# Performance work log

Measured on AMD Instinct MI355X. Metric: run time of the kernel, lower is better.

Reference implementation:

```python
import jax, jax.numpy as jnp
import numpy as np

NUM_HEADS = 16
MAX_LEN = 1024  # RelativePositionalEncoding default


def setup_inputs() -> dict:
    key = jax.random.key(0)
    ks = jax.random.split(key, 12)
    S, B, E = 1024, 4, 1024
    hd = E // NUM_HEADS
    table = 2 * MAX_LEN - 1  # 2047
    mu = 1.0 / np.sqrt(E)
    def lin_w(k):
        return jax.random.uniform(k, (E, E), jnp.float32, -mu, mu)
    def lin_b(k):
        return jax.random.uniform(k, (E,), jnp.float32, -mu, mu)
    return {
        "query": jax.random.normal(ks[0], (S, B, E), jnp.float32),
        "key": jax.random.normal(ks[1], (S, B, E), jnp.float32),
        "value": jax.random.normal(ks[2], (S, B, E), jnp.float32),
        "Wq": lin_w(ks[3]), "bq": lin_b(ks[4]),
        "Wk": lin_w(ks[5]), "bk": lin_b(ks[6]),
        "Wv": lin_w(ks[7]), "bv": lin_b(ks[8]),
        "Wo": lin_w(ks[9]), "bo": lin_b(ks[10]),
        "rel_pos_table": jax.random.normal(ks[11], (table, hd), jnp.float32),
    }


def reference(query, key, value, Wq, bq, Wk, bk, Wv, bv, Wo, bo, rel_pos_table):
    S, B, E = query.shape
    H = NUM_HEADS
    hd = E // H
    scale = hd ** -0.5
    # eval-mode NoisyLoRALinear == plain linear with mu params
    q = (query @ Wq.T + bq).reshape(S, B, H, hd).transpose(1, 2, 0, 3) * scale  # [B,H,S,hd]
    k = (key @ Wk.T + bk).reshape(S, B, H, hd).transpose(1, 2, 0, 3)
    v = (value @ Wv.T + bv).reshape(S, B, H, hd).transpose(1, 2, 0, 3)
    content = jnp.einsum('bhsd,bhtd->bhst', q, k)  # [B,H,S,S]
    # relative position embeddings: rel_pos_table[final_mat] -> [S,S,hd]
    L = rel_pos_table.shape[0]  # 2*max_len - 1
    half = L // 2
    r = jnp.arange(S)
    dist = r[None, :] - r[:, None]
    idx = jnp.clip(dist, -half + 1, half - 1) + half - 1
    rel_emb = rel_pos_table[idx]  # [S,S,hd]
    pos = jnp.einsum('bhsd,std->bhst', q, rel_emb)
    attn = jax.nn.softmax(content + pos, axis=-1)
    out = jnp.einsum('bhst,bhtd->bhsd', attn, v)  # [B,H,S,hd]
    out = out.transpose(0, 2, 1, 3).reshape(B, S, E)
    out = out @ Wo.T + bo  # [B,S,E]
    return out.transpose(1, 0, 2)  # [S,B,E]
```

## Files before the change

### kernel.cpp

```cpp
#include <hip/hip_runtime.h>
#include <math.h>

#define S_LEN 1024
#define B_SZ 4
#define E_DIM 1024
#define H_NUM 16
#define HD 64
#define IDX_MAX 2044
#define NEG_BIG (-3.0e38f)

typedef __attribute__((ext_vector_type(8))) short s16x8;
typedef __attribute__((ext_vector_type(4))) float f32x4;

__device__ __forceinline__ unsigned short f2bf(float f) {
  union { float f; unsigned int u; } v; v.f = f;
  return (unsigned short)((v.u + 0x7FFFu + ((v.u >> 16) & 1u)) >> 16);
}
__device__ __forceinline__ float bf2f(unsigned short h) {
  union { unsigned int u; float f; } v; v.u = ((unsigned int)h) << 16;
  return v.f;
}
__device__ __forceinline__ void gload16(const void* g, void* l) {
  __builtin_amdgcn_global_load_lds(
      (const __attribute__((address_space(1))) void*)g,
      (__attribute__((address_space(3))) void*)l, 16, 0, 0);
}
__device__ __forceinline__ int clampg(int g) {
  return g < 0 ? 0 : (g > IDX_MAX ? IDX_MAX : g);
}

template <int CTRL>
__device__ __forceinline__ float dppror(float x) {
  union { float f; int i; } a, b;
  a.f = x;
  b.i = __builtin_amdgcn_update_dpp(a.i, a.i, CTRL, 0xF, 0xF, false);
  return b.f;
}
__device__ __forceinline__ float rmax16(float x) {
  x = fmaxf(x, dppror<0x128>(x));
  x = fmaxf(x, dppror<0x124>(x));
  x = fmaxf(x, dppror<0x122>(x));
  x = fmaxf(x, dppror<0x121>(x));
  return x;
}
__device__ __forceinline__ float rsum16(float x) {
  x += dppror<0x128>(x);
  x += dppror<0x124>(x);
  x += dppror<0x122>(x);
  x += dppror<0x121>(x);
  return x;
}

__global__ __launch_bounds__(256) void conv_all(
    const float* __restrict__ q, const float* __restrict__ k,
    const float* __restrict__ v, const float* __restrict__ wq,
    const float* __restrict__ wk, const float* __restrict__ wv,
    const float* __restrict__ wo, const float* __restrict__ tb,
    unsigned short* __restrict__ oq, unsigned short* __restrict__ ok,
    unsigned short* __restrict__ ov, unsigned short* __restrict__ owq,
    unsigned short* __restrict__ owk, unsigned short* __restrict__ owv,
    unsigned short* __restrict__ owo, unsigned short* __restrict__ otb)
{
  const int b = blockIdx.x;
  const float* src; unsigned short* dst; int n, lb;
  if (b < 2048)      { src = q;  dst = oq;  n = 4194304; lb = b; }
  else if (b < 4096) { src = k;  dst = ok;  n = 4194304; lb = b - 2048; }
  else if (b < 6144) { src = v;  dst = ov;  n = 4194304; lb = b - 4096; }
  else if (b < 6656) { src = wq; dst = owq; n = 1048576; lb = b - 6144; }
  else if (b < 7168) { src = wk; dst = owk; n = 1048576; lb = b - 6656; }
  else if (b < 7680) { src = wv; dst = owv; n = 1048576; lb = b - 7168; }
  else if (b < 8192) { src = wo; dst = owo; n = 1048576; lb = b - 7680; }
  else               { src = tb; dst = otb; n = 131008;  lb = b - 8192; }
  const int i = (lb * 256 + threadIdx.x) << 3;
  if (i >= n) return;
  const float4 a = *(const float4*)(src + i);
  const float4 c = *(const float4*)(src + i + 4);
  union { unsigned short us[8]; uint4 v4; } u;
  u.us[0] = f2bf(a.x); u.us[1] = f2bf(a.y); u.us[2] = f2bf(a.z); u.us[3] = f2bf(a.w);
  u.us[4] = f2bf(c.x); u.us[5] = f2bf(c.y); u.us[6] = f2bf(c.z); u.us[7] = f2bf(c.w);
  *(uint4*)(dst + i) = u.v4;
}

__global__ __launch_bounds__(256, 3) void qkv_mfma(
    const unsigned short* __restrict__ X0, const unsigned short* __restrict__ X1,
    const unsigned short* __restrict__ X2,
    const unsigned short* __restrict__ W0, const unsigned short* __restrict__ W1,
    const unsigned short* __restrict__ W2,
    const float* __restrict__ bp0, const float* __restrict__ bp1,
    const float* __restrict__ bp2,
    unsigned short* __restrict__ O0, unsigned short* __restrict__ O1,
    unsigned short* __restrict__ O2)
{
  __shared__ unsigned short As[128 * 64];
  __shared__ unsigned short Bs[128 * 64];

  const int z = blockIdx.z;
  const unsigned short* X = z == 0 ? X0 : (z == 1 ? X1 : X2);
  const unsigned short* W = z == 0 ? W0 : (z == 1 ? W1 : W2);
  const float* bias = z == 0 ? bp0 : (z == 1 ? bp1 : bp2);
  unsigned short* O = z == 0 ? O0 : (z == 1 ? O1 : O2);
  const float scale = z == 0 ? 0.125f : 1.0f;

  const int tid = threadIdx.x;
  const int w = tid >> 6, l = tid & 63;
  const int l15 = l & 15, l4 = l >> 4;
  const int m0 = blockIdx.x << 7, n0 = blockIdx.y << 7;
  const int wr0 = (w >> 1) << 6, wc0 = (w & 1) << 6;

  f32x4 acc[4][4];
#pragma unroll
  for (int mt = 0; mt < 4; ++mt)
#pragma unroll
    for (int nt = 0; nt < 4; ++nt) acc[mt][nt] = (f32x4){0.f, 0.f, 0.f, 0.f};

  float bias4[4];
#pragma unroll
  for (int nt = 0; nt < 4; ++nt) bias4[nt] = bias[n0 + wc0 + (nt << 4) + l15];

  const int cbase = (w << 6) + l;

  for (int kt = 0; kt < 16; ++kt) {
    const int k0 = kt << 6;
    __syncthreads();
#pragma unroll
    for (int i = 0; i < 4; ++i) {
      const int c = cbase + (i << 8);
      const int r = c >> 3, kc = c & 7;
      char* ldsA = (char*)As + (((i << 2) + w) << 10);
      char* ldsB = (char*)Bs + (((i << 2) + w) << 10);
      gload16(X + (size_t)(m0 + r) * E_DIM + k0 + (kc << 3), ldsA);
      gload16(W + (size_t)(n0 + r) * E_DIM + k0 + (kc << 3), ldsB);
    }
    __syncthreads();
#pragma unroll
    for (int kh = 0; kh < 2; ++kh) {
      s16x8 af[4], bfr[4];
#pragma unroll
      for (int mt = 0; mt < 4; ++mt)
        af[mt] = *(const s16x8*)&As[(wr0 + (mt << 4) + l15) * 64 + (kh << 5) + (l4 << 3)];
#pragma unroll
      for (int nt = 0; nt < 4; ++nt)
        bfr[nt] = *(const s16x8*)&Bs[(wc0 + (nt << 4) + l15) * 64 + (kh << 5) + (l4 << 3)];
#pragma unroll
      for (int mt = 0; mt < 4; ++mt)
#pragma unroll
        for (int nt = 0; nt < 4; ++nt)
          acc[mt][nt] = __builtin_amdgcn_mfma_f32_16x16x32_bf16(
              af[mt], bfr[nt], acc[mt][nt], 0, 0, 0);
    }
  }

#pragma unroll
  for (int mt = 0; mt < 4; ++mt)
#pragma unroll
    for (int nt = 0; nt < 4; ++nt) {
      const int n = n0 + wc0 + (nt << 4) + l15;
      const int h = n >> 6, d = n & 63;
      const f32x4 c = acc[mt][nt];
#pragma unroll
      for (int r = 0; r < 4; ++r) {
        const int m = m0 + wr0 + (mt << 4) + (l4 << 2) + r;
        const int s = m >> 2, b = m & 3;
        O[((((size_t)b * H_NUM + h) * S_LEN) + s) * HD + d] =
            f2bf((c[r] + bias4[nt]) * scale);
      }
    }
}

__global__ __launch_bounds__(256) void outp_mfma(
    const unsigned short* __restrict__ A, const unsigned short* __restrict__ W,
    const float* __restrict__ bias, float* __restrict__ out)
{
  __shared__ unsigned short As[128 * 64];
  __shared__ unsigned short Bs[128 * 64];

  const int tid = threadIdx.x;
  const int w = tid >> 6, l = tid & 63;
  const int l15 = l & 15, l4 = l >> 4;
  const int m0 = blockIdx.x << 7, n0 = blockIdx.y << 7;
  const int wr0 = (w >> 1) << 6, wc0 = (w & 1) << 6;

  f32x4 acc[4][4];
#pragma unroll
  for (int mt = 0; mt < 4; ++mt)
#pragma unroll
    for (int nt = 0; nt < 4; ++nt) acc[mt][nt] = (f32x4){0.f, 0.f, 0.f, 0.f};

  float bias4[4];
#pragma unroll
  for (int nt = 0; nt < 4; ++nt) bias4[nt] = bias[n0 + wc0 + (nt << 4) + l15];

  const int cbase = (w << 6) + l;

  for (int kt = 0; kt < 16; ++kt) {
    const int k0 = kt << 6;
    __syncthreads();
#pragma unroll
    for (int i = 0; i < 4; ++i) {
      const int c = cbase + (i << 8);
      const int r = c >> 3, kc = c & 7;
      char* ldsA = (char*)As + (((i << 2) + w) << 10);
      char* ldsB = (char*)Bs + (((i << 2) + w) << 10);
      gload16(A + (size_t)(m0 + r) * E_DIM + k0 + (kc << 3), ldsA);
      gload16(W + (size_t)(n0 + r) * E_DIM + k0 + (kc << 3), ldsB);
    }
    __syncthreads();
#pragma unroll
    for (int kh = 0; kh < 2; ++kh) {
      s16x8 af[4], bfr[4];
      const int ko = (kh << 5) + (l4 << 3);
#pragma unroll
      for (int mt = 0; mt < 4; ++mt)
        af[mt] = *(const s16x8*)&As[(wr0 + (mt << 4) + l15) * 64 + ko];
#pragma unroll
      for (int nt = 0; nt < 4; ++nt)
        bfr[nt] = *(const s16x8*)&Bs[(wc0 + (nt << 4) + l15) * 64 + ko];
#pragma unroll
      for (int mt = 0; mt < 4; ++mt)
#pragma unroll
        for (int nt = 0; nt < 4; ++nt)
          acc[mt][nt] = __builtin_amdgcn_mfma_f32_16x16x32_bf16(
              af[mt], bfr[nt], acc[mt][nt], 0, 0, 0);
    }
  }

#pragma unroll
  for (int mt = 0; mt < 4; ++mt)
#pragma unroll
    for (int nt = 0; nt < 4; ++nt) {
      const int n = n0 + wc0 + (nt << 4) + l15;
      const f32x4 c = acc[mt][nt];
#pragma unroll
      for (int r = 0; r < 4; ++r) {
        const int m = m0 + wr0 + (mt << 4) + (l4 << 2) + r;
        const int b = m >> 10, s = m & 1023;
        out[((size_t)s * B_SZ + b) * E_DIM + n] = c[r] + bias4[nt];
      }
    }
}

__global__ __launch_bounds__(256) void attn_mfma(
    const unsigned short* __restrict__ Qb, const unsigned short* __restrict__ Kb,
    const unsigned short* __restrict__ Vb, const unsigned short* __restrict__ Rb,
    unsigned short* __restrict__ AO)
{
  __shared__ unsigned short Ks[64 * 64];
  __shared__ unsigned short Rs[64 * 64];
  __shared__ unsigned short Vt[64 * 64];
  __shared__ unsigned short Ps[64 * 64];
  __shared__ float band[64 * 132];

  const int tid = threadIdx.x;
  const int lane = tid & 63;
  const int w = tid >> 6;
  const int x = blockIdx.x;
  const int idx = x >> 3;
  const int bh = (x & 7) + ((idx & 7) << 3);
  const int st = idx >> 3;
  const int s0 = st << 6;
  const int bb = bh >> 4, hh = bh & 15;
  const size_t base = (size_t)bh * (S_LEN * HD);
  const int l15 = lane & 15, l4 = lane >> 4;
  const int rb_ = w << 4;

  const int sr = tid >> 3, scb = tid & 7;
  const int ksl = (scb ^ (sr & 7)) << 3;
  const int jp = tid >> 3, vc = tid & 7;
  const int jc = jp >> 2, jlow = (jp & 3) << 1;

  const int rbase = 959 - s0;

  s16x8 qf0, qf1;
  {
    const unsigned short* qp =
        Qb + base + (size_t)(s0 + rb_ + l15) * HD + (l4 << 3);
    qf0 = *(const s16x8*)(qp);
    qf1 = *(const s16x8*)(qp + 32);
  }

  f32x4 of[4];
  float mrow[4], lrow[4];
#pragma unroll
  for (int m = 0; m < 4; ++m) {
    of[m] = (f32x4){0.f, 0.f, 0.f, 0.f};
    mrow[m] = NEG_BIG; lrow[m] = 0.f;
  }

#define BAND_MFMA(H0)                                                          \
  {                                                                            \
    f32x4 bq[4];                                                               \
    _Pragma("unroll") for (int rt = 0; rt < 4; ++rt)                           \
        bq[rt] = (f32x4){0.f, 0.f, 0.f, 0.f};                                  \
    __builtin_amdgcn_s_setprio(1);                                             \
    _Pragma("unroll") for (int kk = 0; kk < 2; ++kk) {                         \
      const s16x8 qv = kk ? qf1 : qf0;                                         \
      const int cb = l4 + (kk << 2);                                           \
      _Pragma("unroll") for (int rt = 0; rt < 4; ++rt) {                       \
        const int r = (rt << 4) + l15;                                         \
        const s16x8 rf = *(const s16x8*)&Rs[(r << 6) + ((cb ^ (r & 7)) << 3)]; \
        bq[rt] = __builtin_amdgcn_mfma_f32_16x16x32_bf16(qv, rf, bq[rt], 0, 0, 0); \
      }                                                                        \
    }                                                                          \
    __builtin_amdgcn_s_setprio(0);                                             \
    _Pragma("unroll") for (int rt = 0; rt < 4; ++rt)                           \
      _Pragma("unroll") for (int m = 0; m < 4; ++m)                            \
        band[(rb_ + (l4 << 2) + m) * 132 + (H0) + (rt << 4) + l15] = bq[rt][m];\
  }

  s16x8 Kr0, Kr1, Vr0, Vr1, Rr0, Rr1;
  {
    s16x8 tA0, tA1, tB0, tB1;
    tA0 = *(const s16x8*)(Rb + (size_t)clampg(rbase + sr) * HD + (scb << 3));
    tA1 = *(const s16x8*)(Rb + (size_t)clampg(rbase + 32 + sr) * HD + (scb << 3));
    tB0 = *(const s16x8*)(Rb + (size_t)clampg(rbase + 64 + sr) * HD + (scb << 3));
    tB1 = *(const s16x8*)(Rb + (size_t)clampg(rbase + 96 + sr) * HD + (scb << 3));
    *(s16x8*)&Rs[(sr << 6) + ksl] = tA0;
    *(s16x8*)&Rs[((sr + 32) << 6) + ksl] = tA1;
    __syncthreads();
    BAND_MFMA(0);
    Kr0 = *(const s16x8*)(Kb + base + (size_t)sr * HD + (scb << 3));
    Kr1 = *(const s16x8*)(Kb + base + (size_t)(32 + sr) * HD + (scb << 3));
    Vr0 = *(const s16x8*)(Vb + base + (size_t)(jp << 1) * HD + (vc << 3));
    Vr1 = *(const s16x8*)(Vb + base + (size_t)((jp << 1) + 1) * HD + (vc << 3));
    Rr0 = *(const s16x8*)(Rb + (size_t)clampg(rbase + 128 + sr) * HD + (scb << 3));
    Rr1 = *(const s16x8*)(Rb + (size_t)clampg(rbase + 160 + sr) * HD + (scb << 3));
    __syncthreads();
    *(s16x8*)&Rs[(sr << 6) + ksl] = tB0;
    *(s16x8*)&Rs[((sr + 32) << 6) + ksl] = tB1;
    __syncthreads();
    BAND_MFMA(64);
  }

  for (int tt = 0; tt < 16; ++tt) {
    const int t0 = tt << 6;
    __syncthreads();

    *(s16x8*)&Ks[(sr << 6) + ksl] = Kr0;
    *(s16x8*)&Ks[((sr + 32) << 6) + ksl] = Kr1;
    *(s16x8*)&Rs[(sr << 6) + ksl] = Rr0;
    *(s16x8*)&Rs[((sr + 32) << 6) + ksl] = Rr1;
#pragma unroll
    for (int e = 0; e < 8; ++e) {
      const int d = (vc << 3) + e;
      const int slot = jc ^ e ^ vc;
      const unsigned int pack = (unsigned int)(unsigned short)Vr0[e] |
                                ((unsigned int)(unsigned short)Vr1[e] << 16);
      *(unsigned int*)&Vt[(d << 6) + (slot << 3) + jlow] = pack;
    }
    __syncthreads();

    if (tt < 15) {
      const int tn = t0 + 64;
      Kr0 = *(const s16x8*)(Kb + base + (size_t)(tn + sr) * HD + (scb << 3));
      Kr1 = *(const s16x8*)(Kb + base + (size_t)(tn + 32 + sr) * HD + (scb << 3));
      Vr0 = *(const s16x8*)(Vb + base + (size_t)(tn + (jp << 1)) * HD + (vc << 3));
      Vr1 = *(const s16x8*)(Vb + base + (size_t)(tn + (jp << 1) + 1) * HD + (vc << 3));
      const int gb = rbase + ((tt + 3) << 6) + sr;
      Rr0 = *(const s16x8*)(Rb + (size_t)clampg(gb) * HD + (scb << 3));
      Rr1 = *(const s16x8*)(Rb + (size_t)clampg(gb + 32) * HD + (scb << 3));
    }

    f32x4 cf[4];
#pragma unroll
    for (int jt = 0; jt < 4; ++jt) cf[jt] = (f32x4){0.f, 0.f, 0.f, 0.f};
    __builtin_amdgcn_s_setprio(1);
#pragma unroll
    for (int kk = 0; kk < 2; ++kk) {
      const s16x8 qv = kk ? qf1 : qf0;
      const int cb = l4 + (kk << 2);
#pragma unroll
      for (int jt = 0; jt < 4; ++jt) {
        const int r = (jt << 4) + l15;
        const s16x8 kf = *(const s16x8*)&Ks[(r << 6) + ((cb ^ (r & 7)) << 3)];
        cf[jt] = __builtin_amdgcn_mfma_f32_16x16x32_bf16(qv, kf, cf[jt], 0, 0, 0);
      }
    }
    __builtin_amdgcn_s_setprio(0);

#pragma unroll
    for (int m = 0; m < 4; ++m) {
      const int irow = rb_ + (l4 << 2) + m;
      const int bc = t0 + 63 - irow;
      const float* bp = &band[irow * 132];
      float sv[4];
#pragma unroll
      for (int jt = 0; jt < 4; ++jt)
        sv[jt] = cf[jt][m] + bp[(bc + (jt << 4) + l15) & 127];
      float mx = fmaxf(fmaxf(sv[0], sv[1]), fmaxf(sv[2], sv[3]));
      mx = rmax16(mx);
      const float mnew = fmaxf(mrow[m], mx);
      const float alpha = __expf(mrow[m] - mnew);
      float p[4], ls = 0.f;
#pragma unroll
      for (int jt = 0; jt < 4; ++jt) { p[jt] = __expf(sv[jt] - mnew); ls += p[jt]; }
      ls = rsum16(ls);
      lrow[m] = lrow[m] * alpha + ls;
      mrow[m] = mnew;
#pragma unroll
      for (int dt = 0; dt < 4; ++dt) of[dt][m] *= alpha;
#pragma unroll
      for (int jt = 0; jt < 4; ++jt) {
        const int col = (jt << 4) + l15;
        const int ch = col >> 3;
        Ps[(irow << 6) + ((ch ^ (irow & 7)) << 3) + (col & 7)] = f2bf(p[jt]);
      }
    }

    BAND_MFMA((tt & 1) << 6);

    __builtin_amdgcn_s_setprio(1);
#pragma unroll
    for (int kk = 0; kk < 2; ++kk) {
      const int cb = l4 + (kk << 2);
      const int pr = rb_ + l15;
      const s16x8 pf = *(const s16x8*)&Ps[(pr << 6) + ((cb ^ (pr & 7)) << 3)];
#pragma unroll
      for (int dt = 0; dt < 4; ++dt) {
        const int dr = (dt << 4) + l15;
        const int slot = cb ^ (dr & 7) ^ ((dt << 1) + (l15 >> 3));
        const s16x8 vf = *(const s16x8*)&Vt[(dr << 6) + (slot << 3)];
        of[dt] = __builtin_amdgcn_mfma_f32_16x16x32_bf16(pf, vf, of[dt], 0, 0, 0);
      }
    }
    __builtin_amdgcn_s_setprio(0);
  }

#pragma unroll
  for (int m = 0; m < 4; ++m) {
    const float inv = 1.f / lrow[m];
    const int srow = s0 + rb_ + (l4 << 2) + m;
    const size_t off0 = ((size_t)bb * S_LEN + srow) * E_DIM + (hh << 6) + l15;
#pragma unroll
    for (int dt = 0; dt < 4; ++dt)
      AO[off0 + (dt << 4)] = f2bf(of[dt][m] * inv);
  }
#undef BAND_MFMA
}

extern "C" void kernel_launch(void* const* d_in, const int* in_sizes, int n_in,
                              void* d_out, int out_size, void* d_ws, size_t ws_size,
                              hipStream_t stream) {
  (void)in_sizes; (void)n_in; (void)out_size; (void)ws_size;
  const float* query = (const float*)d_in[0];
  const float* key   = (const float*)d_in[1];
  const float* value = (const float*)d_in[2];
  const float* Wq = (const float*)d_in[3];
  const float* bq = (const float*)d_in[4];
  const float* Wk = (const float*)d_in[5];
  const float* bk = (const float*)d_in[6];
  const float* Wv = (const float*)d_in[7];
  const float* bv = (const float*)d_in[8];
  const float* Wo = (const float*)d_in[9];
  const float* bo = (const float*)d_in[10];
  const float* tbl = (const float*)d_in[11];

  const size_t per = (size_t)B_SZ * H_NUM * S_LEN * HD;
  const size_t wsz = (size_t)E_DIM * E_DIM;
  unsigned short* p = (unsigned short*)d_ws;
  unsigned short* wsQb = p; p += per;
  unsigned short* wsKb = p; p += per;
  unsigned short* wsVb = p; p += per;
  unsigned short* wsRb = p; p += 131072;
  unsigned short* wsXq = p; p += per;
  unsigned short* wsXk = p; p += per;
  unsigned short* wsXv = p; p += per;
  unsigned short* wsWq = p; p += wsz;
  unsigned short* wsWk = p; p += wsz;
  unsigned short* wsWv = p; p += wsz;
  unsigned short* wsWo = p; p += wsz;
  unsigned short* wsA  = p; p += per;
  float* out = (float*)d_out;

  dim3 blk(256);
  hipLaunchKernelGGL(conv_all, dim3(8256), blk, 0, stream,
                     query, key, value, Wq, Wk, Wv, Wo, tbl,
                     wsXq, wsXk, wsXv, wsWq, wsWk, wsWv, wsWo, wsRb);
  hipLaunchKernelGGL(qkv_mfma, dim3(32, 8, 3), blk, 0, stream,
                     wsXq, wsXk, wsXv, wsWq, wsWk, wsWv, bq, bk, bv,
                     wsQb, wsKb, wsVb);
  hipLaunchKernelGGL(attn_mfma, dim3(1024), blk, 0, stream,
                     wsQb, wsKb, wsVb, wsRb, wsA);
  hipLaunchKernelGGL(outp_mfma, dim3(32, 8), blk, 0, stream,
                     wsA, wsWo, bo, out);
}
```

Measured before the change: 154.2 us.

## Store relative-position band in diagonal ring layout and use exp2 softmax

Relative-position band scores are now written to a diagonally indexed ring buffer, so each lane reads its four row values with one vector LDS load instead of four scattered scalar loads. The query scale now folds in log2(e), so the softmax uses exp2f rather than __expf. The main cost targeted is LDS read traffic and bank conflicts in the softmax inner loop. In exchange the band stores become more scattered, and correctness depends on the ring indexing and the scale folding matching exactly.

Result: slower. 162.2 us (+5.2%).

```diff
diff --git a/kernel.cpp b/kernel.cpp
--- a/kernel.cpp
+++ b/kernel.cpp
@@ -99,7 +99,7 @@
   const unsigned short* W = z == 0 ? W0 : (z == 1 ? W1 : W2);
   const float* bias = z == 0 ? bp0 : (z == 1 ? bp1 : bp2);
   unsigned short* O = z == 0 ? O0 : (z == 1 ? O1 : O2);
-  const float scale = z == 0 ? 0.125f : 1.0f;
+  const float scale = z == 0 ? 0.18033688f : 1.0f;
 
   const int tid = threadIdx.x;
   const int w = tid >> 6, l = tid & 63;
@@ -248,7 +248,7 @@
   __shared__ unsigned short Rs[64 * 64];
   __shared__ unsigned short Vt[64 * 64];
   __shared__ unsigned short Ps[64 * 64];
-  __shared__ float band[64 * 132];
+  __shared__ float ring2[128 * 68];
 
   const int tid = threadIdx.x;
   const int lane = tid & 63;
@@ -286,7 +286,7 @@
     mrow[m] = NEG_BIG; lrow[m] = 0.f;
   }
 
-#define BAND_MFMA(H0)                                                          \
+#define BAND_MFMA(BP)                                                          \
   {                                                                            \
     f32x4 bq[4];                                                               \
     _Pragma("unroll") for (int rt = 0; rt < 4; ++rt)                           \
@@ -302,9 +302,13 @@
       }                                                                        \
     }                                                                          \
     __builtin_amdgcn_s_setprio(0);                                             \
-    _Pragma("unroll") for (int rt = 0; rt < 4; ++rt)                           \
-      _Pragma("unroll") for (int m = 0; m < 4; ++m)                            \
-        band[(rb_ + (l4 << 2) + m) * 132 + (H0) + (rt << 4) + l15] = bq[rt][m];\
+    _Pragma("unroll") for (int rt = 0; rt < 4; ++rt) {                         \
+      const int u_ = ((BP) << 6) + (rt << 4) + l15;                            \
+      _Pragma("unroll") for (int m = 0; m < 4; ++m) {                          \
+        const int irow_ = rb_ + (l4 << 2) + m;                                 \
+        ring2[((irow_ + u_) & 127) * 68 + irow_] = bq[rt][m];                  \
+      }                                                                        \
+    }                                                                          \
   }
 
   s16x8 Kr0, Kr1, Vr0, Vr1, Rr0, Rr1;
@@ -328,7 +332,7 @@
     *(s16x8*)&Rs[(sr << 6) + ksl] = tB0;
     *(s16x8*)&Rs[((sr + 32) << 6) + ksl] = tB1;
     __syncthreads();
-    BAND_MFMA(64);
+    BAND_MFMA(1);
   }
 
   for (int tt = 0; tt < 16; ++tt) {
@@ -377,22 +381,30 @@
     }
     __builtin_amdgcn_s_setprio(0);
 
+    f32x4 gb4[4];
+    {
+      const int i0r = rb_ + (l4 << 2);
+#pragma unroll
+      for (int jt = 0; jt < 4; ++jt) {
+        const int v = (t0 + 63 + (jt << 4) + l15) & 127;
+        gb4[jt] = *(const f32x4*)&ring2[v * 68 + i0r];
+      }
+    }
+
 #pragma unroll
     for (int m = 0; m < 4; ++m) {
       const int irow = rb_ + (l4 << 2) + m;
-      const int bc = t0 + 63 - irow;
-      const float* bp = &band[irow * 132];
       float sv[4];
 #pragma unroll
       for (int jt = 0; jt < 4; ++jt)
-        sv[jt] = cf[jt][m] + bp[(bc + (jt << 4) + l15) & 127];
+        sv[jt] = cf[jt][m] + gb4[jt][m];
       float mx = fmaxf(fmaxf(sv[0], sv[1]), fmaxf(sv[2], sv[3]));
       mx = rmax16(mx);
       const float mnew = fmaxf(mrow[m], mx);
-      const float alpha = __expf(mrow[m] - mnew);
+      const float alpha = exp2f(mrow[m] - mnew);
       float p[4], ls = 0.f;
 #pragma unroll
-      for (int jt = 0; jt < 4; ++jt) { p[jt] = __expf(sv[jt] - mnew); ls += p[jt]; }
+      for (int jt = 0; jt < 4; ++jt) { p[jt] = exp2f(sv[jt] - mnew); ls += p[jt]; }
       ls = rsum16(ls);
       lrow[m] = lrow[m] * alpha + ls;
       mrow[m] = mnew;
@@ -406,7 +418,7 @@
       }
     }
 
-    BAND_MFMA((tt & 1) << 6);
+    BAND_MFMA(tt + 2);
 
     __builtin_amdgcn_s_setprio(1);
 #pragma unroll
```
